# Optimization experiments

Hardware: AMD Instinct MI355X
Metric: run time of the kernel (lower is better)

## Reference

```python
import jax, jax.numpy as jnp
import numpy as np

D_MODEL = 512
N_HEADS = 8
HEAD_DIM = D_MODEL // N_HEADS
D_FF = 2048
EPS = 1e-5


def layer_norm(x, gamma, beta):
    mu = jnp.mean(x, axis=-1, keepdims=True)
    var = jnp.mean((x - mu) ** 2, axis=-1, keepdims=True)
    return (x - mu) * jax.lax.rsqrt(var + EPS) * gamma + beta


def setup_inputs() -> dict:
    key = jax.random.key(0)
    ks = jax.random.split(key, 17)
    B, S = 2, 2048
    s_in = 1.0 / np.sqrt(D_MODEL)
    s_ff = 1.0 / np.sqrt(D_FF)
    return {
        "x": jax.random.normal(ks[0], (B, S, D_MODEL), jnp.float32),
        "Wq": jax.random.normal(ks[1], (D_MODEL, D_MODEL), jnp.float32) * s_in,
        "bq": jnp.zeros((D_MODEL,), jnp.float32),
        "Wk": jax.random.normal(ks[2], (D_MODEL, D_MODEL), jnp.float32) * s_in,
        "bk": jnp.zeros((D_MODEL,), jnp.float32),
        "Wv": jax.random.normal(ks[3], (D_MODEL, D_MODEL), jnp.float32) * s_in,
        "bv": jnp.zeros((D_MODEL,), jnp.float32),
        "Wo": jax.random.normal(ks[4], (D_MODEL, D_MODEL), jnp.float32) * s_in,
        "bo": jnp.zeros((D_MODEL,), jnp.float32),
        "W1": jax.random.normal(ks[5], (D_MODEL, D_FF), jnp.float32) * s_in,
        "b1": jnp.zeros((D_FF,), jnp.float32),
        "W2": jax.random.normal(ks[6], (D_FF, D_MODEL), jnp.float32) * s_ff,
        "b2": jnp.zeros((D_MODEL,), jnp.float32),
        "g1": jnp.ones((D_MODEL,), jnp.float32),
        "be1": jnp.zeros((D_MODEL,), jnp.float32),
        "g2": jnp.ones((D_MODEL,), jnp.float32),
        "be2": jnp.zeros((D_MODEL,), jnp.float32),
    }


def reference(x, Wq, bq, Wk, bk, Wv, bv, Wo, bo, W1, b1, W2, b2, g1, be1, g2, be2):
    B, S, _ = x.shape
    # projections + split heads -> [B, H, S, Dh]
    def heads(t):
        return t.reshape(B, S, N_HEADS, HEAD_DIM).transpose(0, 2, 1, 3)
    q = heads(x @ Wq + bq)
    k = heads(x @ Wk + bk)
    v = heads(x @ Wv + bv)
    # explicit scaled dot-product attention (full [B,H,S,S] scores as in source)
    scores = jnp.einsum('bhqd,bhkd->bhqk', q, k) / np.sqrt(HEAD_DIM).astype(np.float32)
    attn = jax.nn.softmax(scores, axis=-1)
    ctx = jnp.einsum('bhqk,bhkd->bhqd', attn, v)
    ctx = ctx.transpose(0, 2, 1, 3).reshape(B, S, D_MODEL)
    attn_out = ctx @ Wo + bo
    # post-norm residual 1
    h = layer_norm(x + attn_out, g1, be1)
    # FFN
    ff = jax.nn.relu(h @ W1 + b1) @ W2 + b2
    # post-norm residual 2
    return layer_norm(h + ff, g2, be2)
```

## Files before the change

### kernel.cpp

```cpp
#include <hip/hip_runtime.h>
#include <cmath>

#define D_MODEL 512
#define N_HEADS 8
#define HEAD_DIM 64
#define D_FF 2048
#define SEQ 2048
#define BATCH 2
#define MROWS (BATCH * SEQ)

typedef __attribute__((ext_vector_type(8))) short short8;
typedef __attribute__((ext_vector_type(4))) float float4v;
typedef unsigned short ushort_t;

static __device__ __forceinline__ ushort_t f2bf(float f) {
    union { float f; unsigned u; } v; v.f = f;
    unsigned r = (v.u + 0x7FFFu + ((v.u >> 16) & 1u)) >> 16;
    return (ushort_t)r;
}
static __device__ __forceinline__ ushort_t f2bf_trunc(float f) {
    union { float f; unsigned u; } v; v.f = f;
    return (ushort_t)(v.u >> 16);
}

static __device__ __forceinline__ void gload16(const void* g, void* l) {
    __builtin_amdgcn_global_load_lds(
        (__attribute__((address_space(1))) void*)(unsigned long long)g,
        (__attribute__((address_space(3))) void*)(unsigned)(unsigned long long)l,
        16, 0, 0);
}

__global__ __launch_bounds__(256) void prep_k(
    const float* __restrict__ x,
    const float* __restrict__ Wq, const float* __restrict__ Wk,
    const float* __restrict__ Wv, const float* __restrict__ Wo,
    const float* __restrict__ W1, const float* __restrict__ W2,
    ushort_t* __restrict__ xb,
    ushort_t* __restrict__ WqkvT, ushort_t* __restrict__ WoT,
    ushort_t* __restrict__ W1T, ushort_t* __restrict__ W2T)
{
    int tile = blockIdx.x;
    if (tile >= 3072) {
        int i = (tile - 3072) * 256 + threadIdx.x;
        float4 f = ((const float4*)x)[i];
        ushort4 o;
        o.x = f2bf(f.x); o.y = f2bf(f.y); o.z = f2bf(f.z); o.w = f2bf(f.w);
        ((ushort4*)xb)[i] = o;
        return;
    }
    const float* src; ushort_t* dst; int Kd, Nd, tloc;
    if (tile < 1024) {
        int wsel = tile >> 8; tloc = tile & 255; Kd = 512; Nd = 512;
        if (wsel == 0)      { src = Wq; dst = WqkvT; }
        else if (wsel == 1) { src = Wk; dst = WqkvT + (size_t)512 * 512; }
        else if (wsel == 2) { src = Wv; dst = WqkvT + (size_t)1024 * 512; }
        else                { src = Wo; dst = WoT; }
    } else if (tile < 2048) { tloc = tile - 1024; Kd = 512;  Nd = 2048; src = W1; dst = W1T; }
    else                    { tloc = tile - 2048; Kd = 2048; Nd = 512;  src = W2; dst = W2T; }
    int tn = Nd >> 5;
    int k0 = (tloc / tn) << 5, n0 = (tloc % tn) << 5;
    __shared__ float tl[32][33];
    int c = threadIdx.x & 31, r = threadIdx.x >> 5;
    #pragma unroll
    for (int i = 0; i < 4; ++i)
        tl[r + i * 8][c] = src[(size_t)(k0 + r + i * 8) * Nd + n0 + c];
    __syncthreads();
    #pragma unroll
    for (int i = 0; i < 4; ++i)
        dst[(size_t)(n0 + r + i * 8) * Kd + k0 + c] = f2bf(tl[c][r + i * 8]);
}

template <int MODE>
__global__ __launch_bounds__(256) void gemm_std_k(
    const ushort_t* __restrict__ A, const ushort_t* __restrict__ BT,
    const float* __restrict__ bias, void* __restrict__ Cv,
    int N, int K, int Klen, size_t zstride)
{
    __shared__ ushort_t As[64 * 128];
    __shared__ ushort_t Bs[128 * 128];

    const int t = threadIdx.x;
    const int w = t >> 6, lane = t & 63, l16 = lane & 15, quad = lane >> 4;
    const int m0 = blockIdx.y * 64;
    const int n0 = blockIdx.x * 128;
    const int kbase = blockIdx.z * Klen;
    const int mbase = (w >> 1) * 32;
    const int nbase = (w & 1) * 64;
    const int lrow = lane >> 4;
    const int lchunk = lane & 15;

    float4v acc[2][4];
    #pragma unroll
    for (int mt = 0; mt < 2; ++mt)
        #pragma unroll
        for (int nt = 0; nt < 4; ++nt)
            acc[mt][nt] = (float4v){0.f, 0.f, 0.f, 0.f};

    for (int ks = kbase; ks < kbase + Klen; ks += 128) {
        __syncthreads();
        for (int c = w; c < 16; c += 4) {
            int rl = c * 4 + lrow;
            gload16(A + (size_t)(m0 + rl) * K + ks + ((lchunk ^ (rl & 7)) << 3),
                    &As[c * 512]);
        }
        for (int c = w; c < 32; c += 4) {
            int rl = c * 4 + lrow;
            gload16(BT + (size_t)(n0 + rl) * K + ks + ((lchunk ^ (rl & 7)) << 3),
                    &Bs[c * 512]);
        }
        __syncthreads();

        #pragma unroll
        for (int co = 0; co < 4; ++co) {
            const int poff = (((co * 4 + quad) ^ (l16 & 7)) << 3);
            short8 af[2], bf8[4];
            #pragma unroll
            for (int mt = 0; mt < 2; ++mt)
                af[mt] = *(const short8*)&As[(mbase + mt * 16 + l16) * 128 + poff];
            #pragma unroll
            for (int nt = 0; nt < 4; ++nt)
                bf8[nt] = *(const short8*)&Bs[(nbase + nt * 16 + l16) * 128 + poff];
            #pragma unroll
            for (int mt = 0; mt < 2; ++mt)
                #pragma unroll
                for (int nt = 0; nt < 4; ++nt)
                    acc[mt][nt] = __builtin_amdgcn_mfma_f32_16x16x32_bf16(
                        af[mt], bf8[nt], acc[mt][nt], 0, 0, 0);
        }
    }

    float* Cf = (float*)Cv + blockIdx.z * zstride;
    #pragma unroll
    for (int mt = 0; mt < 2; ++mt) {
        #pragma unroll
        for (int nt = 0; nt < 4; ++nt) {
            int gcol = n0 + nbase + nt * 16 + l16;
            float b = (MODE == 2) ? 0.f : bias[gcol];
            #pragma unroll
            for (int r = 0; r < 4; ++r) {
                int grow = m0 + mbase + mt * 16 + quad * 4 + r;
                float v = acc[mt][nt][r] + b;
                if (MODE == 1) v = fmaxf(v, 0.f);
                if (MODE == 1) ((ushort_t*)Cv)[(size_t)grow * N + gcol] = f2bf(v);
                else           Cf[(size_t)grow * N + gcol] = v;
            }
        }
    }
}

__global__ __launch_bounds__(256) void gemm_qkv_k(
    const ushort_t* __restrict__ A, const ushort_t* __restrict__ BT,
    const float* __restrict__ bq, const float* __restrict__ bk,
    const float* __restrict__ bv,
    ushort_t* __restrict__ Qb, ushort_t* __restrict__ Kb,
    ushort_t* __restrict__ VTb)
{
    __shared__ ushort_t As[64 * 128];
    __shared__ ushort_t Bs[128 * 128];

    const int t = threadIdx.x;
    const int w = t >> 6, lane = t & 63, l16 = lane & 15, quad = lane >> 4;
    const int m0 = blockIdx.y * 64;
    const int n0 = blockIdx.x * 128;
    const int mbase = (w >> 1) * 32;
    const int nbase = (w & 1) * 64;
    const int lrow = lane >> 4;
    const int lchunk = lane & 15;
    const int K = 512;

    float4v acc[2][4];
    #pragma unroll
    for (int mt = 0; mt < 2; ++mt)
        #pragma unroll
        for (int nt = 0; nt < 4; ++nt)
            acc[mt][nt] = (float4v){0.f, 0.f, 0.f, 0.f};

    for (int ks = 0; ks < 512; ks += 128) {
        __syncthreads();
        for (int c = w; c < 16; c += 4) {
            int rl = c * 4 + lrow;
            gload16(A + (size_t)(m0 + rl) * K + ks + ((lchunk ^ (rl & 7)) << 3),
                    &As[c * 512]);
        }
        for (int c = w; c < 32; c += 4) {
            int rl = c * 4 + lrow;
            gload16(BT + (size_t)(n0 + rl) * K + ks + ((lchunk ^ (rl & 7)) << 3),
                    &Bs[c * 512]);
        }
        __syncthreads();

        #pragma unroll
        for (int co = 0; co < 4; ++co) {
            const int poff = (((co * 4 + quad) ^ (l16 & 7)) << 3);
            short8 af[2], bf8[4];
            #pragma unroll
            for (int mt = 0; mt < 2; ++mt)
                af[mt] = *(const short8*)&As[(mbase + mt * 16 + l16) * 128 + poff];
            #pragma unroll
            for (int nt = 0; nt < 4; ++nt)
                bf8[nt] = *(const short8*)&Bs[(nbase + nt * 16 + l16) * 128 + poff];
            #pragma unroll
            for (int mt = 0; mt < 2; ++mt)
                #pragma unroll
                for (int nt = 0; nt < 4; ++nt)
                    acc[mt][nt] = __builtin_amdgcn_mfma_f32_16x16x32_bf16(
                        af[mt], bf8[nt], acc[mt][nt], 0, 0, 0);
        }
    }

    const int tsel = n0 >> 9;
    const float* bias = (tsel == 0) ? bq : (tsel == 1) ? bk : bv;
    const float scl = (tsel == 0) ? 0.18033688f : 1.0f;
    ushort_t* dst = (tsel == 0) ? Qb : Kb;

    #pragma unroll
    for (int mt = 0; mt < 2; ++mt) {
        #pragma unroll
        for (int nt = 0; nt < 4; ++nt) {
            int gcol = n0 + nbase + nt * 16 + l16;
            int lcol = gcol - (tsel << 9);
            int h = lcol >> 6, dh = lcol & 63;
            float b = bias[lcol];
            #pragma unroll
            for (int r = 0; r < 4; ++r) {
                int grow = m0 + mbase + mt * 16 + quad * 4 + r;
                int bb = grow >> 11, s = grow & 2047;
                float v = (acc[mt][nt][r] + b) * scl;
                if (tsel < 2)
                    dst[(((size_t)(bb * N_HEADS + h)) * SEQ + s) * HEAD_DIM + dh] = f2bf(v);
                else
                    VTb[(((size_t)(bb * N_HEADS + h)) * HEAD_DIM + dh) * SEQ + s] = f2bf(v);
            }
        }
    }
}

__global__ __launch_bounds__(256) void attn_mfma_k(
    const ushort_t* __restrict__ Qg, const ushort_t* __restrict__ Kg,
    const ushort_t* __restrict__ VTg,
    ushort_t* __restrict__ Ctx)
{
    __shared__ __align__(16) ushort_t Kbuf[4][64 * 64];
    __shared__ __align__(16) ushort_t Vbuf[4][64 * 64];
    __shared__ __align__(16) ushort_t Ps[4][16 * 64];

    const int bh = blockIdx.x;
    const int q0 = blockIdx.y * 64;
    const int t = threadIdx.x;
    const int w = t >> 6;
    const int lane = t & 63;
    const int l16 = lane & 15;
    const int quad = lane >> 4;
    const int qbase = q0 + w * 16;
    const float NM2 = -14.4269504f;

    const int r0 = t >> 3;
    const int r1 = r0 + 32;
    const int g0 = (t & 7) ^ (r0 & 7);
    const int g1 = (t & 7) ^ (r1 & 7);
    const size_t kgrow = (size_t)bh * SEQ;
    const size_t vgrow = (size_t)bh * HEAD_DIM;

#define ATTN_STAGE(b, kb)                                                       \
    {                                                                           \
        gload16(Kg + (kgrow + (kb) + r0) * HEAD_DIM + g0 * 8, &Kbuf[b][w * 512]);          \
        gload16(Kg + (kgrow + (kb) + r1) * HEAD_DIM + g1 * 8, &Kbuf[b][2048 + w * 512]);   \
        gload16(VTg + (vgrow + r0) * SEQ + (kb) + g0 * 8, &Vbuf[b][w * 512]);              \
        gload16(VTg + (vgrow + r1) * SEQ + (kb) + g1 * 8, &Vbuf[b][2048 + w * 512]);       \
    }

    short8 aq[2];
    {
        const ushort_t* qp = Qg + ((size_t)bh * SEQ + qbase + l16) * HEAD_DIM + quad * 8;
        aq[0] = *(const short8*)(qp);
        aq[1] = *(const short8*)(qp + 32);
    }

    const short8 ones8 = {(short)0x3F80, (short)0x3F80, (short)0x3F80, (short)0x3F80,
                          (short)0x3F80, (short)0x3F80, (short)0x3F80, (short)0x3F80};

    float4v o[4] = {};
    float4v ol = {};

    ATTN_STAGE(0, 0)
    ATTN_STAGE(1, 64)

    for (int i = 0; i < 32; ++i) {
        const int cur = i & 3;
        if (i < 30) {
            ATTN_STAGE((i + 2) & 3, (i + 2) * 64)
            asm volatile("s_waitcnt vmcnt(8)" ::: "memory");
        } else if (i == 30) {
            asm volatile("s_waitcnt vmcnt(4)" ::: "memory");
        } else {
            asm volatile("s_waitcnt vmcnt(0)" ::: "memory");
        }
        asm volatile("s_barrier" ::: "memory");

        const ushort_t* Kc = Kbuf[cur];
        const ushort_t* Vc = Vbuf[cur];

        float4v s[4];
        #pragma unroll
        for (int nt = 0; nt < 4; ++nt)
            s[nt] = (float4v){NM2, NM2, NM2, NM2};

        __builtin_amdgcn_s_setprio(1);
        #pragma unroll
        for (int c = 0; c < 2; ++c) {
            const int poff = (((c * 4 + quad) ^ (l16 & 7)) << 3);
            #pragma unroll
            for (int nt = 0; nt < 4; ++nt) {
                short8 bk8 = *(const short8*)&Kc[(nt * 16 + l16) * 64 + poff];
                s[nt] = __builtin_amdgcn_mfma_f32_16x16x32_bf16(aq[c], bk8, s[nt], 0, 0, 0);
            }
        }
        __builtin_amdgcn_s_setprio(0);

        #pragma unroll
        for (int nt = 0; nt < 4; ++nt)
            #pragma unroll
            for (int r = 0; r < 4; ++r)
                s[nt][r] = exp2f(s[nt][r]);

        #pragma unroll
        for (int nt = 0; nt < 4; ++nt)
            #pragma unroll
            for (int r = 0; r < 4; ++r) {
                int row = quad * 4 + r;
                int key = nt * 16 + l16;
                Ps[w][row * 64 + (((key >> 3) ^ (row & 7)) << 3) + (key & 7)] =
                    f2bf_trunc(s[nt][r]);
            }
        asm volatile("s_waitcnt lgkmcnt(0)" ::: "memory");

        __builtin_amdgcn_s_setprio(1);
        #pragma unroll
        for (int c = 0; c < 2; ++c) {
            short8 ap = *(const short8*)&Ps[w][l16 * 64 + ((((c << 2) + quad) ^ (l16 & 7)) << 3)];
            const int poff = (((c * 4 + quad) ^ (l16 & 7)) << 3);
            #pragma unroll
            for (int dt = 0; dt < 4; ++dt) {
                short8 bv8 = *(const short8*)&Vc[(dt * 16 + l16) * 64 + poff];
                o[dt] = __builtin_amdgcn_mfma_f32_16x16x32_bf16(ap, bv8, o[dt], 0, 0, 0);
            }
            ol = __builtin_amdgcn_mfma_f32_16x16x32_bf16(ap, ones8, ol, 0, 0, 0);
        }
        __builtin_amdgcn_s_setprio(0);
    }
#undef ATTN_STAGE

    const int bb = bh >> 3, hh = bh & 7;
    #pragma unroll
    for (int r = 0; r < 4; ++r) {
        int q = qbase + quad * 4 + r;
        float inv = 1.0f / ol[r];
        #pragma unroll
        for (int dt = 0; dt < 4; ++dt)
            Ctx[((size_t)(bb * SEQ + q)) * D_MODEL + hh * HEAD_DIM + dt * 16 + l16] =
                f2bf(o[dt][r] * inv);
    }
}

__global__ __launch_bounds__(256) void wo_ln_k(
    const ushort_t* __restrict__ Ctx,
    const ushort_t* __restrict__ WoT,
    const float* __restrict__ x,
    const float* __restrict__ bo,
    const float* __restrict__ gam, const float* __restrict__ bet,
    float* __restrict__ Hh, ushort_t* __restrict__ Hhb)
{
    __shared__ __align__(16) ushort_t As[16 * 512];
    __shared__ __align__(16) ushort_t Bs[2][512 * 64];
    __shared__ float red[2][4][16];

    const int t = threadIdx.x;
    const int w = t >> 6, lane = t & 63, l16 = lane & 15, quad = lane >> 4;
    const int m0 = blockIdx.x * 16;
    const int K = 512;

    #pragma unroll
    for (int p = 0; p < 4; ++p) {
        int row = p * 4 + w;
        int g = (lane & 56) | ((lane & 7) ^ (row & 7));
        gload16(Ctx + (size_t)(m0 + row) * K + g * 8, &As[row * 512]);
    }

#define WOLN_STAGE_B(b, ks)                                                     \
    {                                                                           \
        _Pragma("unroll")                                                       \
        for (int c = 0; c < 16; ++c) {                                          \
            int row = c * 32 + (t >> 3);                                        \
            int g = (t & 7) ^ (row & 7);                                        \
            gload16(WoT + (size_t)row * K + (ks) * 64 + g * 8,                  \
                    &Bs[b][c * 2048 + w * 512]);                                \
        }                                                                       \
    }

    float4v acc[8];
    #pragma unroll
    for (int nt = 0; nt < 8; ++nt) acc[nt] = (float4v){0.f, 0.f, 0.f, 0.f};

    WOLN_STAGE_B(0, 0)

    for (int ks = 0; ks < 8; ++ks) {
        const int cur = ks & 1;
        if (ks < 7) {
            WOLN_STAGE_B(cur ^ 1, ks + 1)
            asm volatile("s_waitcnt vmcnt(16)" ::: "memory");
        } else {
            asm volatile("s_waitcnt vmcnt(0)" ::: "memory");
        }
        asm volatile("s_barrier" ::: "memory");

        #pragma unroll
        for (int c = 0; c < 2; ++c) {
            const int poff = (((c * 4 + quad) ^ (l16 & 7)) << 3);
            short8 af = *(const short8*)&As[l16 * 512 + ks * 64 + poff];
            #pragma unroll
            for (int nt = 0; nt < 8; ++nt) {
                short8 bv = *(const short8*)&Bs[cur][(w * 128 + nt * 16 + l16) * 64 + poff];
                acc[nt] = __builtin_amdgcn_mfma_f32_16x16x32_bf16(af, bv, acc[nt], 0, 0, 0);
            }
        }
        asm volatile("s_barrier" ::: "memory");
    }
#undef WOLN_STAGE_B

    float v[8][4];
    float s[4] = {0.f, 0.f, 0.f, 0.f}, ss[4] = {0.f, 0.f, 0.f, 0.f};
    #pragma unroll
    for (int nt = 0; nt < 8; ++nt) {
        int col = w * 128 + nt * 16 + l16;
        float b = bo[col];
        #pragma unroll
        for (int r = 0; r < 4; ++r) {
            int grow = m0 + quad * 4 + r;
            float val = acc[nt][r] + b + x[(size_t)grow * D_MODEL + col];
            v[nt][r] = val;
            s[r] += val;
            ss[r] += val * val;
        }
    }
    #pragma unroll
    for (int r = 0; r < 4; ++r) {
        #pragma unroll
        for (int m = 1; m < 16; m <<= 1) {
            s[r]  += __shfl_xor(s[r], m);
            ss[r] += __shfl_xor(ss[r], m);
        }
    }
    if (l16 == 0) {
        #pragma unroll
        for (int r = 0; r < 4; ++r) {
            red[0][w][quad * 4 + r] = s[r];
            red[1][w][quad * 4 + r] = ss[r];
        }
    }
    __syncthreads();
    #pragma unroll
    for (int r = 0; r < 4; ++r) {
        int lrow = quad * 4 + r;
        float S  = red[0][0][lrow] + red[0][1][lrow] + red[0][2][lrow] + red[0][3][lrow];
        float SS = red[1][0][lrow] + red[1][1][lrow] + red[1][2][lrow] + red[1][3][lrow];
        float mu  = S * (1.0f / D_MODEL);
        float var = SS * (1.0f / D_MODEL) - mu * mu;
        float inv = rsqrtf(var + 1e-5f);
        int grow = m0 + lrow;
        #pragma unroll
        for (int nt = 0; nt < 8; ++nt) {
            int col = w * 128 + nt * 16 + l16;
            float o = (v[nt][r] - mu) * inv * gam[col] + bet[col];
            Hh[(size_t)grow * D_MODEL + col] = o;
            Hhb[(size_t)grow * D_MODEL + col] = f2bf(o);
        }
    }
}

template <int WRITE_BF>
__global__ __launch_bounds__(256) void add_ln_k(
    const float* __restrict__ X, const float* __restrict__ P0,
    const float* __restrict__ P1, const float* __restrict__ bias,
    const float* __restrict__ gam, const float* __restrict__ bet,
    float* __restrict__ O, ushort_t* __restrict__ Ob)
{
    const int row = blockIdx.x;
    const int t = threadIdx.x;
    const size_t ro = (size_t)row * D_MODEL;

    float v0 = X[ro + t]       + P0[ro + t]       + P1[ro + t]       + bias[t];
    float v1 = X[ro + t + 256] + P0[ro + t + 256] + P1[ro + t + 256] + bias[t + 256];
    float s = v0 + v1;
    float ss = v0 * v0 + v1 * v1;
    #pragma unroll
    for (int off = 32; off > 0; off >>= 1) {
        s  += __shfl_down(s, off);
        ss += __shfl_down(ss, off);
    }
    __shared__ float sb[4], ssb[4];
    if ((t & 63) == 0) { sb[t >> 6] = s; ssb[t >> 6] = ss; }
    __syncthreads();
    float S  = sb[0] + sb[1] + sb[2] + sb[3];
    float SS = ssb[0] + ssb[1] + ssb[2] + ssb[3];
    float mu  = S * (1.0f / D_MODEL);
    float var = SS * (1.0f / D_MODEL) - mu * mu;
    float inv = rsqrtf(var + 1e-5f);
    float o0 = (v0 - mu) * inv * gam[t] + bet[t];
    float o1 = (v1 - mu) * inv * gam[t + 256] + bet[t + 256];
    O[ro + t]       = o0;
    O[ro + t + 256] = o1;
    if (WRITE_BF) {
        Ob[ro + t]       = f2bf(o0);
        Ob[ro + t + 256] = f2bf(o1);
    }
}

extern "C" void kernel_launch(void* const* d_in, const int* in_sizes, int n_in,
                              void* d_out, int out_size, void* d_ws, size_t ws_size,
                              hipStream_t stream)
{
    const float* x   = (const float*)d_in[0];
    const float* Wq  = (const float*)d_in[1];
    const float* bq  = (const float*)d_in[2];
    const float* Wk  = (const float*)d_in[3];
    const float* bk  = (const float*)d_in[4];
    const float* Wv  = (const float*)d_in[5];
    const float* bv  = (const float*)d_in[6];
    const float* Wo  = (const float*)d_in[7];
    const float* bo  = (const float*)d_in[8];
    const float* W1  = (const float*)d_in[9];
    const float* b1  = (const float*)d_in[10];
    const float* W2  = (const float*)d_in[11];
    const float* b2  = (const float*)d_in[12];
    const float* g1  = (const float*)d_in[13];
    const float* be1 = (const float*)d_in[14];
    const float* g2  = (const float*)d_in[15];
    const float* be2 = (const float*)d_in[16];
    float* out = (float*)d_out;
    float* ws  = (float*)d_ws;

    ushort_t* WoT   = (ushort_t*)(ws);
    ushort_t* W1T   = (ushort_t*)(ws + 131072);
    ushort_t* W2T   = (ushort_t*)(ws + 655360);
    ushort_t* WqkvT = (ushort_t*)(ws + 1179648);
    ushort_t* xb    = (ushort_t*)(ws + 1572864);
    ushort_t* Qb    = (ushort_t*)(ws + 2621440);
    ushort_t* Kb    = (ushort_t*)(ws + 3670016);
    ushort_t* VTb   = (ushort_t*)(ws + 4718592);
    ushort_t* Ctx   = (ushort_t*)(ws + 5767168);
    float*    Hh    = ws + 6881280;
    float*    P0    = ws + 8978432;
    float*    P1    = ws + 11075584;
    ushort_t* FF1   = (ushort_t*)(ws + 1572864);
    ushort_t* Hhb   = (ushort_t*)(ws + 5767168);

    prep_k<<<5120, 256, 0, stream>>>(x, Wq, Wk, Wv, Wo, W1, W2, xb, WqkvT, WoT, W1T, W2T);

    gemm_qkv_k<<<dim3(12, 64), 256, 0, stream>>>(xb, WqkvT, bq, bk, bv, Qb, Kb, VTb);

    attn_mfma_k<<<dim3(16, 32), 256, 0, stream>>>(Qb, Kb, VTb, Ctx);

    wo_ln_k<<<256, 256, 0, stream>>>(Ctx, WoT, x, bo, g1, be1, Hh, Hhb);

    gemm_std_k<1><<<dim3(16, 64), 256, 0, stream>>>(
        Hhb, W1T, b1, FF1, 2048, 512, 512, 0);

    gemm_std_k<2><<<dim3(4, 64, 2), 256, 0, stream>>>(
        FF1, W2T, nullptr, P0, 512, 2048, 1024, (size_t)MROWS * D_MODEL);

    add_ln_k<0><<<4096, 256, 0, stream>>>(Hh, P0, P1, b2, g2, be2, out, (ushort_t*)nullptr);
}
```

Baseline: 209.5 us.

## Fuse W2 GEMM with residual add and final LayerNorm

Replaces the split-K W2 GEMM plus separate add+LayerNorm kernel with one kernel where each block computes 16 full output rows over the whole K dimension and applies bias, residual and LayerNorm in registers. This removes writing and rereading two fp32 partial buffers and one launch. In exchange there are fewer blocks, large shared memory per block, and every block reloads the full W2 slice, raising L2 traffic and lowering parallelism.

```diff
diff --git a/kernel.cpp b/kernel.cpp
--- a/kernel.cpp
+++ b/kernel.cpp
@@ -477,41 +477,116 @@
     }
 }
 
-template <int WRITE_BF>
-__global__ __launch_bounds__(256) void add_ln_k(
-    const float* __restrict__ X, const float* __restrict__ P0,
-    const float* __restrict__ P1, const float* __restrict__ bias,
+__global__ __launch_bounds__(256) void w2_ln_k(
+    const ushort_t* __restrict__ FF1g,
+    const ushort_t* __restrict__ W2Tg,
+    const float* __restrict__ Hh,
+    const float* __restrict__ b2,
     const float* __restrict__ gam, const float* __restrict__ bet,
-    float* __restrict__ O, ushort_t* __restrict__ Ob)
+    float* __restrict__ out)
 {
-    const int row = blockIdx.x;
+    __shared__ __align__(16) ushort_t As[2][16 * 64];
+    __shared__ __align__(16) ushort_t Bs[2][512 * 64];
+    __shared__ float red[2][4][16];
+
     const int t = threadIdx.x;
-    const size_t ro = (size_t)row * D_MODEL;
-
-    float v0 = X[ro + t]       + P0[ro + t]       + P1[ro + t]       + bias[t];
-    float v1 = X[ro + t + 256] + P0[ro + t + 256] + P1[ro + t + 256] + bias[t + 256];
-    float s = v0 + v1;
-    float ss = v0 * v0 + v1 * v1;
-    #pragma unroll
-    for (int off = 32; off > 0; off >>= 1) {
-        s  += __shfl_down(s, off);
-        ss += __shfl_down(ss, off);
-    }
-    __shared__ float sb[4], ssb[4];
-    if ((t & 63) == 0) { sb[t >> 6] = s; ssb[t >> 6] = ss; }
+    const int w = t >> 6, lane = t & 63, l16 = lane & 15, quad = lane >> 4;
+    const int m0 = blockIdx.x * 16;
+    const int K = 2048;
+
+#define W2_STAGE(b, ks)                                                         \
+    {                                                                           \
+        if (lane < 32) {                                                        \
+            int cid = w * 32 + lane;                                            \
+            int arow = cid >> 3;                                                \
+            int ag = (cid & 7) ^ (arow & 7);                                    \
+            gload16(FF1g + (size_t)(m0 + arow) * K + (ks) * 64 + ag * 8,        \
+                    &As[b][w * 256]);                                           \
+        }                                                                       \
+        _Pragma("unroll")                                                       \
+        for (int c = 0; c < 16; ++c) {                                          \
+            int brow = c * 32 + (t >> 3);                                       \
+            int bg = (t & 7) ^ (brow & 7);                                      \
+            gload16(W2Tg + (size_t)brow * K + (ks) * 64 + bg * 8,               \
+                    &Bs[b][c * 2048 + w * 512]);                                \
+        }                                                                       \
+    }
+
+    float4v acc[8];
+    #pragma unroll
+    for (int nt = 0; nt < 8; ++nt) acc[nt] = (float4v){0.f, 0.f, 0.f, 0.f};
+
+    W2_STAGE(0, 0)
+
+    for (int ks = 0; ks < 32; ++ks) {
+        const int cur = ks & 1;
+        if (ks < 31) {
+            W2_STAGE(cur ^ 1, ks + 1)
+            asm volatile("s_waitcnt vmcnt(17)" ::: "memory");
+        } else {
+            asm volatile("s_waitcnt vmcnt(0)" ::: "memory");
+        }
+        asm volatile("s_barrier" ::: "memory");
+
+        #pragma unroll
+        for (int c = 0; c < 2; ++c) {
+            const int poff = (((c * 4 + quad) ^ (l16 & 7)) << 3);
+            short8 af = *(const short8*)&As[cur][l16 * 64 + poff];
+            #pragma unroll
+            for (int nt = 0; nt < 8; ++nt) {
+                short8 bv = *(const short8*)&Bs[cur][(w * 128 + nt * 16 + l16) * 64 + poff];
+                acc[nt] = __builtin_amdgcn_mfma_f32_16x16x32_bf16(af, bv, acc[nt], 0, 0, 0);
+            }
+        }
+        asm volatile("s_barrier" ::: "memory");
+    }
+#undef W2_STAGE
+
+    float v[8][4];
+    float s[4] = {0.f, 0.f, 0.f, 0.f}, ss[4] = {0.f, 0.f, 0.f, 0.f};
+    #pragma unroll
+    for (int nt = 0; nt < 8; ++nt) {
+        int col = w * 128 + nt * 16 + l16;
+        float b = b2[col];
+        #pragma unroll
+        for (int r = 0; r < 4; ++r) {
+            int grow = m0 + quad * 4 + r;
+            float val = acc[nt][r] + b + Hh[(size_t)grow * D_MODEL + col];
+            v[nt][r] = val;
+            s[r] += val;
+            ss[r] += val * val;
+        }
+    }
+    #pragma unroll
+    for (int r = 0; r < 4; ++r) {
+        #pragma unroll
+        for (int m = 1; m < 16; m <<= 1) {
+            s[r]  += __shfl_xor(s[r], m);
+            ss[r] += __shfl_xor(ss[r], m);
+        }
+    }
+    if (l16 == 0) {
+        #pragma unroll
+        for (int r = 0; r < 4; ++r) {
+            red[0][w][quad * 4 + r] = s[r];
+            red[1][w][quad * 4 + r] = ss[r];
+        }
+    }
     __syncthreads();
-    float S  = sb[0] + sb[1] + sb[2] + sb[3];
-    float SS = ssb[0] + ssb[1] + ssb[2] + ssb[3];
-    float mu  = S * (1.0f / D_MODEL);
-    float var = SS * (1.0f / D_MODEL) - mu * mu;
-    float inv = rsqrtf(var + 1e-5f);
-    float o0 = (v0 - mu) * inv * gam[t] + bet[t];
-    float o1 = (v1 - mu) * inv * gam[t + 256] + bet[t + 256];
-    O[ro + t]       = o0;
-    O[ro + t + 256] = o1;
-    if (WRITE_BF) {
-        Ob[ro + t]       = f2bf(o0);
-        Ob[ro + t + 256] = f2bf(o1);
+    #pragma unroll
+    for (int r = 0; r < 4; ++r) {
+        int lrow = quad * 4 + r;
+        float S  = red[0][0][lrow] + red[0][1][lrow] + red[0][2][lrow] + red[0][3][lrow];
+        float SS = red[1][0][lrow] + red[1][1][lrow] + red[1][2][lrow] + red[1][3][lrow];
+        float mu  = S * (1.0f / D_MODEL);
+        float var = SS * (1.0f / D_MODEL) - mu * mu;
+        float inv = rsqrtf(var + 1e-5f);
+        int grow = m0 + lrow;
+        #pragma unroll
+        for (int nt = 0; nt < 8; ++nt) {
+            int col = w * 128 + nt * 16 + l16;
+            out[(size_t)grow * D_MODEL + col] = (v[nt][r] - mu) * inv * gam[col] + bet[col];
+        }
     }
 }
 
@@ -549,8 +624,6 @@
     ushort_t* VTb   = (ushort_t*)(ws + 4718592);
     ushort_t* Ctx   = (ushort_t*)(ws + 5767168);
     float*    Hh    = ws + 6881280;
-    float*    P0    = ws + 8978432;
-    float*    P1    = ws + 11075584;
     ushort_t* FF1   = (ushort_t*)(ws + 1572864);
     ushort_t* Hhb   = (ushort_t*)(ws + 5767168);
 
@@ -565,8 +638,5 @@
     gemm_std_k<1><<<dim3(16, 64), 256, 0, stream>>>(
         Hhb, W1T, b1, FF1, 2048, 512, 512, 0);
 
-    gemm_std_k<2><<<dim3(4, 64, 2), 256, 0, stream>>>(
-        FF1, W2T, nullptr, P0, 512, 2048, 1024, (size_t)MROWS * D_MODEL);
-
-    add_ln_k<0><<<4096, 256, 0, stream>>>(Hh, P0, P1, b2, g2, be2, out, (ushort_t*)nullptr);
-}
+    w2_ln_k<<<256, 256, 0, stream>>>(FF1, W2T, Hh, b2, g2, be2, out);
+}
```

New measurement: 216.2 us. +3.2%, slower.

## Keep attention probabilities in registers by transposing QK^T MFMA operands

Applied to the files above, without the earlier changes.

Swaps the A/B operands of the QK^T MFMA so each lane holds a transposed score fragment. The exponentiated scores can then be packed directly into the A operand of the PV MFMA instead of round-tripping through shared memory. This removes the per-iteration LDS stores, the lgkmcnt wait and the reload of P. In exchange, V is now read as two 8-byte halves per fragment with a permuted key order, and lgkmcnt(0) is added to the loop waits.

```diff
diff --git a/kernel.cpp b/kernel.cpp
--- a/kernel.cpp
+++ b/kernel.cpp
@@ -10,6 +10,7 @@
 #define MROWS (BATCH * SEQ)
 
 typedef __attribute__((ext_vector_type(8))) short short8;
+typedef __attribute__((ext_vector_type(4))) short short4v;
 typedef __attribute__((ext_vector_type(4))) float float4v;
 typedef unsigned short ushort_t;
 
@@ -242,7 +243,6 @@
 {
     __shared__ __align__(16) ushort_t Kbuf[4][64 * 64];
     __shared__ __align__(16) ushort_t Vbuf[4][64 * 64];
-    __shared__ __align__(16) ushort_t Ps[4][16 * 64];
 
     const int bh = blockIdx.x;
     const int q0 = blockIdx.y * 64;
@@ -285,15 +285,20 @@
     ATTN_STAGE(0, 0)
     ATTN_STAGE(1, 64)
 
+    const int vq_lo0 = (((quad >> 1))     ^ (l16 & 7)) * 8 + (quad & 1) * 4;
+    const int vq_hi0 = ((2 + (quad >> 1)) ^ (l16 & 7)) * 8 + (quad & 1) * 4;
+    const int vq_lo1 = ((4 + (quad >> 1)) ^ (l16 & 7)) * 8 + (quad & 1) * 4;
+    const int vq_hi1 = ((6 + (quad >> 1)) ^ (l16 & 7)) * 8 + (quad & 1) * 4;
+
     for (int i = 0; i < 32; ++i) {
         const int cur = i & 3;
         if (i < 30) {
             ATTN_STAGE((i + 2) & 3, (i + 2) * 64)
-            asm volatile("s_waitcnt vmcnt(8)" ::: "memory");
+            asm volatile("s_waitcnt vmcnt(8) lgkmcnt(0)" ::: "memory");
         } else if (i == 30) {
-            asm volatile("s_waitcnt vmcnt(4)" ::: "memory");
+            asm volatile("s_waitcnt vmcnt(4) lgkmcnt(0)" ::: "memory");
         } else {
-            asm volatile("s_waitcnt vmcnt(0)" ::: "memory");
+            asm volatile("s_waitcnt vmcnt(0) lgkmcnt(0)" ::: "memory");
         }
         asm volatile("s_barrier" ::: "memory");
 
@@ -312,7 +317,7 @@
             #pragma unroll
             for (int nt = 0; nt < 4; ++nt) {
                 short8 bk8 = *(const short8*)&Kc[(nt * 16 + l16) * 64 + poff];
-                s[nt] = __builtin_amdgcn_mfma_f32_16x16x32_bf16(aq[c], bk8, s[nt], 0, 0, 0);
+                s[nt] = __builtin_amdgcn_mfma_f32_16x16x32_bf16(bk8, aq[c], s[nt], 0, 0, 0);
             }
         }
         __builtin_amdgcn_s_setprio(0);
@@ -323,28 +328,29 @@
             for (int r = 0; r < 4; ++r)
                 s[nt][r] = exp2f(s[nt][r]);
 
-        #pragma unroll
-        for (int nt = 0; nt < 4; ++nt)
-            #pragma unroll
-            for (int r = 0; r < 4; ++r) {
-                int row = quad * 4 + r;
-                int key = nt * 16 + l16;
-                Ps[w][row * 64 + (((key >> 3) ^ (row & 7)) << 3) + (key & 7)] =
-                    f2bf_trunc(s[nt][r]);
+        __builtin_amdgcn_s_setprio(1);
+        #pragma unroll
+        for (int v = 0; v < 2; ++v) {
+            short8 af;
+            af[0] = (short)f2bf_trunc(s[2 * v][0]);
+            af[1] = (short)f2bf_trunc(s[2 * v][1]);
+            af[2] = (short)f2bf_trunc(s[2 * v][2]);
+            af[3] = (short)f2bf_trunc(s[2 * v][3]);
+            af[4] = (short)f2bf_trunc(s[2 * v + 1][0]);
+            af[5] = (short)f2bf_trunc(s[2 * v + 1][1]);
+            af[6] = (short)f2bf_trunc(s[2 * v + 1][2]);
+            af[7] = (short)f2bf_trunc(s[2 * v + 1][3]);
+            const int lo_c = v ? vq_lo1 : vq_lo0;
+            const int hi_c = v ? vq_hi1 : vq_hi0;
+            #pragma unroll
+            for (int dt = 0; dt < 4; ++dt) {
+                const int rb = (dt * 16 + l16) * 64;
+                short4v lo = *(const short4v*)&Vc[rb + lo_c];
+                short4v hi = *(const short4v*)&Vc[rb + hi_c];
+                short8 bv8 = {lo[0], lo[1], lo[2], lo[3], hi[0], hi[1], hi[2], hi[3]};
+                o[dt] = __builtin_amdgcn_mfma_f32_16x16x32_bf16(af, bv8, o[dt], 0, 0, 0);
             }
-        asm volatile("s_waitcnt lgkmcnt(0)" ::: "memory");
-
-        __builtin_amdgcn_s_setprio(1);
-        #pragma unroll
-        for (int c = 0; c < 2; ++c) {
-            short8 ap = *(const short8*)&Ps[w][l16 * 64 + ((((c << 2) + quad) ^ (l16 & 7)) << 3)];
-            const int poff = (((c * 4 + quad) ^ (l16 & 7)) << 3);
-            #pragma unroll
-            for (int dt = 0; dt < 4; ++dt) {
-                short8 bv8 = *(const short8*)&Vc[(dt * 16 + l16) * 64 + poff];
-                o[dt] = __builtin_amdgcn_mfma_f32_16x16x32_bf16(ap, bv8, o[dt], 0, 0, 0);
-            }
-            ol = __builtin_amdgcn_mfma_f32_16x16x32_bf16(ap, ones8, ol, 0, 0, 0);
+            ol = __builtin_amdgcn_mfma_f32_16x16x32_bf16(af, ones8, ol, 0, 0, 0);
         }
         __builtin_amdgcn_s_setprio(0);
     }
@@ -407,9 +413,9 @@
         const int cur = ks & 1;
         if (ks < 7) {
             WOLN_STAGE_B(cur ^ 1, ks + 1)
-            asm volatile("s_waitcnt vmcnt(16)" ::: "memory");
+            asm volatile("s_waitcnt vmcnt(16) lgkmcnt(0)" ::: "memory");
         } else {
-            asm volatile("s_waitcnt vmcnt(0)" ::: "memory");
+            asm volatile("s_waitcnt vmcnt(0) lgkmcnt(0)" ::: "memory");
         }
         asm volatile("s_barrier" ::: "memory");
 
```

Result: no change. 209.4 us (-0.1%).
